# Optimization experiments

Measured on AMD Instinct MI355X. Metric: run time of the kernel, lower is better.

## Reference

```python
import jax, jax.numpy as jnp
import numpy as np

N_USERS = 70000
N_ITEMS = 30000
N_NODES = N_USERS + N_ITEMS
R = 3          # n_relations (hard-coded to 3 in original forward)
D = 64         # emb_dim
L = 2          # n_layers
E = 1_600_000  # nnz per relation adjacency


def setup_inputs() -> dict:
    key = jax.random.key(0)
    ks = jax.random.split(key, 11)
    s = 0.05  # xavier-ish scale
    return {
        'user_emb': jax.random.normal(ks[0], (N_USERS, D), jnp.float32) * s,
        'item_emb': jax.random.normal(ks[1], (N_ITEMS, D), jnp.float32) * s,
        'rel_emb':  jax.random.normal(ks[2], (R, D), jnp.float32) * s,
        'W_gc':     jax.random.normal(ks[3], (L, D, D), jnp.float32) * s,
        'W_rel':    jax.random.normal(ks[4], (L, D, D), jnp.float32) * s,
        'gru_w':    jax.random.normal(ks[5], (R, D, D), jnp.float32) * s,
        'gru_b':    jax.random.normal(ks[6], (R, D), jnp.float32) * s,
        'tra':      jax.random.normal(ks[7], (2, 2 * D), jnp.float32) * s,
        # normalized sparse adjacency values (~1/degree)
        'adj_vals': jax.random.uniform(ks[8], (R, E), jnp.float32) / 16.0,
        'adj_rows': jax.random.randint(ks[9], (R, E), 0, N_NODES, dtype=jnp.int32),
        'adj_cols': jax.random.randint(ks[10], (R, E), 0, N_NODES, dtype=jnp.int32),
    }


def reference(user_emb, item_emb, rel_emb, W_gc, W_rel, gru_w, gru_b, tra,
              adj_vals, adj_rows, adj_cols):
    # ego: [N, R, D] (same embedding replicated per relation channel)
    ego = jnp.broadcast_to(
        jnp.concatenate([user_emb, item_emb], axis=0)[:, None, :],
        (N_NODES, R, D))
    all_emb = ego
    rela = [rel_emb]  # per-layer relation embeddings [R, D]
    inv_sqrt = 1.0 / jnp.sqrt(jnp.float32(128.0))  # hard-coded in source

    for k in range(L):
        embs = []
        for i in range(R):  # small fixed relation loop
            # sparse adj @ ego[:, i, :] via gather + segment_sum
            msgs = ego[adj_cols[i], i, :] * adj_vals[i][:, None]        # [E, D]
            prop = jax.ops.segment_sum(msgs, adj_rows[i],
                                       num_segments=N_NODES)           # [N, D]
            embs.append(jax.nn.leaky_relu((prop * rela[k][i]) @ W_gc[k]))
        est = jnp.stack(embs, axis=1)                                   # [N, R, D]
        att = jax.nn.softmax(
            jnp.einsum('nrd,nsd->nrs', est, est) * inv_sqrt, axis=2)
        ego = jnp.einsum('nrs,nsd->nrd', att, est)
        # dropout rate 0.0 (eval) -> identity
        all_emb = all_emb + ego
        rela.append(rela[k] @ W_rel[k])

    att = jax.nn.softmax(jnp.einsum('nrd,nsd->nrs', all_emb, all_emb), axis=2)
    mid = jnp.einsum('nrs,nsd->nrd', att, all_emb)
    final = jnp.stack([all_emb[:, 0, :], all_emb[:, 1, :], mid[:, -1, :]],
                      axis=1) / (L + 1)                                  # [N, 3, D]
    u = final[:N_USERS]
    i_emb = jnp.concatenate(
        [final[N_USERS:], jnp.zeros((1, R, D), final.dtype)], axis=0)

    aux1 = u[:, 0, :] * (u[:, 0, :] @ gru_w[0] + gru_b[0])
    aux2 = u[:, 1, :] * (u[:, 1, :] @ gru_w[1] + gru_b[1])
    tgt = u[:, 2, :] * (u[:, 2, :] @ gru_w[2] + gru_b[2])
    score1 = jnp.concatenate([tgt, aux1], axis=1) @ tra[0]               # [N_u]
    score2 = jnp.concatenate([tgt, aux2], axis=1) @ tra[1]               # [N_u]

    rela_out = jnp.mean(jnp.stack(rela, axis=0), axis=0)                 # [R, D]
    return (u, i_emb, rela_out, score1, score2)
```

## Files before the change

### kernel.cpp

```cpp
#include <hip/hip_runtime.h>
#include <hip/hip_bf16.h>

#define N_USERS 70000
#define N_ITEMS 30000
#define N_NODES 100000
#define RD 192
#define EE 1600000
#define NE3 4800000
#define M3 300000
#define NSUB 98
#define NBUCK 294

#define OFF_U    0
#define OFF_I    13440000
#define OFF_IZ   19200000
#define OFF_RELA 19200192
#define OFF_S1   19200384
#define OFF_S2   19270384

typedef __hip_bfloat16 bf16;
typedef unsigned long long u64;
typedef __attribute__((ext_vector_type(8))) short short8;
typedef __attribute__((ext_vector_type(8))) unsigned short ushort8;
typedef __attribute__((ext_vector_type(4))) float f32x4;

__device__ __forceinline__ float b2f(bf16 v) { return __bfloat162float(v); }

union bfbits { bf16 b; unsigned short u; };

__device__ __forceinline__ float bits2f(unsigned short u) {
  bfbits x; x.u = u; return b2f(x.b);
}
__device__ __forceinline__ unsigned short f2bits(float f) {
  bfbits x; x.b = __float2bfloat16(f); return x.u;
}

__device__ __forceinline__ float loadf(const void* p, int i, bool f32) {
  return f32 ? ((const float*)p)[i] : b2f(((const bf16*)p)[i]);
}
__device__ __forceinline__ void storef(void* p, int i, float v, bool f32) {
  if (f32) ((float*)p)[i] = v;
  else ((bf16*)p)[i] = __float2bfloat16(v);
}

__device__ __forceinline__ float wave_sum(float v) {
#pragma unroll
  for (int off = 32; off >= 1; off >>= 1) v += __shfl_xor(v, off, 64);
  return v;
}

__global__ void detect_kernel(const unsigned short* __restrict__ ue,
                              int* __restrict__ flag) {
  __shared__ int s;
  int t = threadIdx.x;
  if (t == 0) s = 0;
  __syncthreads();
  int big = 0;
  for (int j = t; j < 8192; j += 256) {
    int e = (ue[j] >> 7) & 0xFF;
    if (e >= 127) big = 1;
  }
  if (big) atomicOr(&s, 1);
  __syncthreads();
  if (t == 0) *flag = s;
}

__global__ void zero_row_kernel(void* out, const int* __restrict__ flag) {
  bool f32 = *flag != 0;
  storef(out, OFF_IZ + (int)threadIdx.x, 0.f, f32);
}

__global__ void rela_kernel(const void* __restrict__ rel_emb,
                            const void* __restrict__ W_rel,
                            const int* __restrict__ flag,
                            float* __restrict__ rela_f, void* out) {
  bool f32 = *flag != 0;
  __shared__ float r0s[192], r1s[192];
  int t = threadIdx.x;
  int i = t >> 6, d = t & 63;
  float r0 = loadf(rel_emb, t, f32);
  r0s[t] = r0;
  __syncthreads();
  float acc = 0.f;
  for (int k = 0; k < 64; ++k)
    acc += r0s[i * 64 + k] * loadf(W_rel, k * 64 + d, f32);
  r1s[t] = acc;
  __syncthreads();
  float acc2 = 0.f;
  for (int k = 0; k < 64; ++k)
    acc2 += r1s[i * 64 + k] * loadf(W_rel, 4096 + k * 64 + d, f32);
  rela_f[t] = r0;
  rela_f[192 + t] = acc;
  rela_f[384 + t] = acc2;
  storef(out, OFF_RELA + t, (r0 + acc + acc2) * (1.f / 3.f), f32);
}

__global__ __launch_bounds__(256) void init_kernel(
    const void* __restrict__ user_emb, const void* __restrict__ item_emb,
    const int* __restrict__ flag, bf16* __restrict__ ego0) {
  bool f32 = *flag != 0;
  int idx4 = blockIdx.x * 256 + threadIdx.x;
  if (idx4 >= N_NODES * RD / 4) return;
  int idx = idx4 << 2;
  int n = idx / RD;
  int rd = idx - n * RD;
  int d = rd & 63;
  const void* src;
  int off;
  if (n < N_USERS) { src = user_emb; off = n * 64 + d; }
  else             { src = item_emb; off = (n - N_USERS) * 64 + d; }
  ushort4 o;
  if (f32) {
    float4 fv = *(const float4*)((const float*)src + off);
    o.x = f2bits(fv.x); o.y = f2bits(fv.y); o.z = f2bits(fv.z); o.w = f2bits(fv.w);
  } else {
    o = *(const ushort4*)((const unsigned short*)src + off);
  }
  *(ushort4*)(ego0 + idx) = o;
}

__global__ __launch_bounds__(256) void bhist_kernel(
    const int* __restrict__ rows, int* __restrict__ bcnt) {
  __shared__ int h[NBUCK];
  int t = threadIdx.x;
  for (int j = t; j < NBUCK; j += 256) h[j] = 0;
  __syncthreads();
  int base = blockIdx.x * 4096;
  int m = min(4096, NE3 - base);
  for (int j = t; j < m; j += 256) {
    int idx = base + j;
    int i = idx / EE;
    int r = rows[idx];
    atomicAdd(&h[i * NSUB + (r >> 10)], 1);
  }
  __syncthreads();
  for (int j = t; j < NBUCK; j += 256)
    if (h[j]) atomicAdd(&bcnt[j], h[j]);
}

__global__ __launch_bounds__(512) void bscan_kernel(
    const int* __restrict__ bcnt, int* __restrict__ gcursor,
    int* __restrict__ bbase) {
  __shared__ int s[512];
  int t = threadIdx.x;
  int x = (t < NBUCK) ? bcnt[t] : 0;
  s[t] = x;
  __syncthreads();
  for (int off = 1; off < 512; off <<= 1) {
    int y = (t >= off) ? s[t - off] : 0;
    __syncthreads();
    s[t] += y;
    __syncthreads();
  }
  if (t < NBUCK) {
    int e = s[t] - x;
    gcursor[t] = e;
    bbase[t] = e;
  }
}

__global__ __launch_bounds__(256) void passA_kernel(
    const int* __restrict__ rows, const int* __restrict__ cols,
    const void* __restrict__ vals, const int* __restrict__ flag,
    int* __restrict__ gcursor, u64* __restrict__ abuf) {
  bool f32 = *flag != 0;
  __shared__ u64 pk[4096];
  __shared__ unsigned short bk[4096];
  __shared__ int cnt[NBUCK], pos[NBUCK], gbase[NBUCK];
  int t = threadIdx.x;
  for (int j = t; j < NBUCK; j += 256) { cnt[j] = 0; pos[j] = 0; }
  __syncthreads();
  int base = blockIdx.x * 4096;
  int m = min(4096, NE3 - base);
  for (int j = t; j < m; j += 256) {
    int idx = base + j;
    int i = idx / EE;
    int r = rows[idx];
    int c = cols[idx];
    unsigned short vb =
        f32 ? f2bits(((const float*)vals)[idx])
            : ((const unsigned short*)vals)[idx];
    int sub = r >> 10;
    int b = i * NSUB + sub;
    pk[j] = ((u64)(r & 1023) << 48) | ((u64)(unsigned)c << 16) | vb;
    bk[j] = (unsigned short)b;
    atomicAdd(&cnt[b], 1);
  }
  __syncthreads();
  for (int j = t; j < NBUCK; j += 256)
    if (cnt[j] > 0) gbase[j] = atomicAdd(&gcursor[j], cnt[j]);
  __syncthreads();
  for (int j = t; j < m; j += 256) {
    int b = bk[j];
    int p = atomicAdd(&pos[b], 1);
    abuf[gbase[b] + p] = pk[j];
  }
}

__global__ __launch_bounds__(256) void passB_kernel(
    const u64* __restrict__ abuf, const int* __restrict__ bbase,
    const int* __restrict__ bcnt, int* __restrict__ offs,
    int* __restrict__ counts, int2* __restrict__ sedge) {
  __shared__ int hist[1024];
  __shared__ int s[256];
  int b = blockIdx.x;
  int rel = b / NSUB, sub = b - rel * NSUB;
  int r0 = sub << 10;
  int nr = min(1024, N_NODES - r0);
  int gi = rel * N_NODES + r0;
  int t = threadIdx.x;
  for (int j = t; j < 1024; j += 256) hist[j] = 0;
  __syncthreads();
  int start = bbase[b];
  int cnt = bcnt[b];
  int end = start + cnt;
  for (int e = start + t; e < end; e += 256)
    atomicAdd(&hist[(int)(abuf[e] >> 48)], 1);
  __syncthreads();
  int j0 = t << 2;
  int a0 = hist[j0], a1 = hist[j0 + 1], a2 = hist[j0 + 2], a3 = hist[j0 + 3];
  int lsum = a0 + a1 + a2 + a3;
  s[t] = lsum;
  __syncthreads();
  for (int off = 1; off < 256; off <<= 1) {
    int y = (t >= off) ? s[t - off] : 0;
    __syncthreads();
    s[t] += y;
    __syncthreads();
  }
  int o0 = start + s[t] - lsum;
  int o1 = o0 + a0, o2 = o1 + a1, o3 = o2 + a2;
  hist[j0] = o0; hist[j0 + 1] = o1; hist[j0 + 2] = o2; hist[j0 + 3] = o3;
  if (j0 < nr) {
    *(int4*)(offs + gi + j0) = make_int4(o0, o1, o2, o3);
    *(int4*)(counts + gi + j0) = make_int4(a0, a1, a2, a3);
  }
  __syncthreads();
  int rbase = rel * 128;
  for (int e = start + t; e < end; e += 256) {
    u64 w = abuf[e];
    int rowlo = (int)(w >> 48);
    int c = (int)((w >> 16) & 0x3FFFF);
    float v = bits2f((unsigned short)(w & 0xFFFF));
    int p = atomicAdd(&hist[rowlo], 1);
    int2 eo; eo.x = c * 384 + rbase; eo.y = __float_as_int(v);
    sedge[p] = eo;
  }
}

__global__ __launch_bounds__(256, 8) void gather_kernel(
    const int2* __restrict__ sedge, const int* __restrict__ counts,
    const int* __restrict__ offs, const bf16* __restrict__ ego,
    bf16* __restrict__ prop) {
  int wave = threadIdx.x >> 6;
  int n = blockIdx.x * 4 + wave;
  int rel = blockIdx.y;
  int seg = rel * N_NODES + n;
  int lane = threadIdx.x & 63;
  int g = lane >> 3;
  int d8 = lane & 7;
  unsigned voff = (unsigned)(d8 << 4);
  int base = __builtin_amdgcn_readfirstlane(offs[seg]);
  int cnt = __builtin_amdgcn_readfirstlane(counts[seg]);
  const char* egob = (const char*)ego;
  float a0 = 0.f, a1 = 0.f, a2 = 0.f, a3 = 0.f;
  float a4 = 0.f, a5 = 0.f, a6 = 0.f, a7 = 0.f;
#define ACCUM(dv, vv)                                          \
  do {                                                         \
    a0 = fmaf(__int_as_float((dv).x << 16), (vv), a0);         \
    a1 = fmaf(__int_as_float((dv).x & 0xffff0000u), (vv), a1); \
    a2 = fmaf(__int_as_float((dv).y << 16), (vv), a2);         \
    a3 = fmaf(__int_as_float((dv).y & 0xffff0000u), (vv), a3); \
    a4 = fmaf(__int_as_float((dv).z << 16), (vv), a4);         \
    a5 = fmaf(__int_as_float((dv).z & 0xffff0000u), (vv), a5); \
    a6 = fmaf(__int_as_float((dv).w << 16), (vv), a6);         \
    a7 = fmaf(__int_as_float((dv).w & 0xffff0000u), (vv), a7); \
  } while (0)
  int cm = cnt - 1;
  int nb = (cnt + 15) >> 4;
  int j = 0;
  if (nb & 1) {
    int iA = min(g, cm), iB = min(8 + g, cm);
    int2 h0 = sedge[base + iA];
    int2 h1 = sedge[base + iB];
    uint4 dA = *(const uint4*)(egob + ((unsigned)h0.x + voff));
    uint4 dB = *(const uint4*)(egob + ((unsigned)h1.x + voff));
    float v0 = (g < cnt) ? __int_as_float(h0.y) : 0.f;
    float v1 = (8 + g < cnt) ? __int_as_float(h1.y) : 0.f;
    ACCUM(dA, v0);
    ACCUM(dB, v1);
    j = 16;
  }
  int e16 = nb << 4;
  for (; j < e16; j += 32) {
    int iA0 = min(j + g, cm),      iB0 = min(j + 8 + g, cm);
    int iA1 = min(j + 16 + g, cm), iB1 = min(j + 24 + g, cm);
    int2 h0a = sedge[base + iA0];
    int2 h1a = sedge[base + iB0];
    int2 h0b = sedge[base + iA1];
    int2 h1b = sedge[base + iB1];
    uint4 dA = *(const uint4*)(egob + ((unsigned)h0a.x + voff));
    uint4 dB = *(const uint4*)(egob + ((unsigned)h1a.x + voff));
    uint4 dC = *(const uint4*)(egob + ((unsigned)h0b.x + voff));
    uint4 dD = *(const uint4*)(egob + ((unsigned)h1b.x + voff));
    float v0 = (j + g < cnt) ? __int_as_float(h0a.y) : 0.f;
    float v1 = (j + 8 + g < cnt) ? __int_as_float(h1a.y) : 0.f;
    float v2 = (j + 16 + g < cnt) ? __int_as_float(h0b.y) : 0.f;
    float v3 = (j + 24 + g < cnt) ? __int_as_float(h1b.y) : 0.f;
    ACCUM(dA, v0);
    ACCUM(dB, v1);
    ACCUM(dC, v2);
    ACCUM(dD, v3);
  }
#undef ACCUM
#pragma unroll
  for (int off = 8; off <= 32; off <<= 1) {
    a0 += __shfl_xor(a0, off, 64);
    a1 += __shfl_xor(a1, off, 64);
    a2 += __shfl_xor(a2, off, 64);
    a3 += __shfl_xor(a3, off, 64);
    a4 += __shfl_xor(a4, off, 64);
    a5 += __shfl_xor(a5, off, 64);
    a6 += __shfl_xor(a6, off, 64);
    a7 += __shfl_xor(a7, off, 64);
  }
  if (g == 0) {
    uint4 o;
    o.x = (unsigned)f2bits(a0) | ((unsigned)f2bits(a1) << 16);
    o.y = (unsigned)f2bits(a2) | ((unsigned)f2bits(a3) << 16);
    o.z = (unsigned)f2bits(a4) | ((unsigned)f2bits(a5) << 16);
    o.w = (unsigned)f2bits(a6) | ((unsigned)f2bits(a7) << 16);
    *(uint4*)((char*)prop + (size_t)(n * RD + rel * 64) * 2 + voff) = o;
  }
}

__device__ __forceinline__ float attn_row(float a, float b, float c,
                                          float e0, float e1, float e2) {
  float m = fmaxf(a, fmaxf(b, c));
  float w0 = __expf(a - m), w1 = __expf(b - m), w2 = __expf(c - m);
  float inv = 1.f / (w0 + w1 + w2);
  return (w0 * e0 + w1 * e1 + w2 * e2) * inv;
}

__global__ __launch_bounds__(256, 4) void transform_attn_kernel(
    const bf16* __restrict__ prop, const float* __restrict__ rela_k,
    const void* __restrict__ Wgc, int wgc_off, const int* __restrict__ flag,
    bf16* __restrict__ ego_out) {
  bool f32 = *flag != 0;
  __shared__ __align__(16) unsigned short est_t[64 * 198];
  int t = threadIdx.x, lane = t & 63, wave = t >> 6;
  int quad = lane >> 4, m = lane & 15;
  int wcol = wave * 16 + m;
  short8 b0, b1;
#pragma unroll
  for (int j = 0; j < 8; ++j) {
    int k0 = quad * 8 + j;
    b0[j] = (short)f2bits(loadf(Wgc, wgc_off + k0 * 64 + wcol, f32));
    b1[j] = (short)f2bits(loadf(Wgc, wgc_off + (k0 + 32) * 64 + wcol, f32));
  }
  float relv0[16], relv1[16], relv2[16];
#pragma unroll
  for (int j = 0; j < 8; ++j) {
    int k0 = quad * 8 + j;
    relv0[j] = rela_k[k0];        relv0[8 + j] = rela_k[32 + k0];
    relv1[j] = rela_k[64 + k0];   relv1[8 + j] = rela_k[96 + k0];
    relv2[j] = rela_k[128 + k0];  relv2[8 + j] = rela_k[160 + k0];
  }
  int n0 = blockIdx.x * 64;
  int row0 = n0 * 3;
#pragma unroll
  for (int tr = 0; tr < 12; ++tr) {
    int rl = tr * 16 + m;
    int row = row0 + rl;
    int row_c = row < M3 ? row : 0;
    int i = rl % 3;
    const ushort8* pp = (const ushort8*)(prop + (size_t)row_c * 64 + quad * 8);
    ushort8 x0 = pp[0];
    ushort8 x1 = pp[4];
    short8 a0, a1;
#pragma unroll
    for (int j = 0; j < 8; ++j) {
      float r0 = (i == 0) ? relv0[j] : (i == 1 ? relv1[j] : relv2[j]);
      float r1 = (i == 0) ? relv0[8 + j] : (i == 1 ? relv1[8 + j] : relv2[8 + j]);
      a0[j] = (short)f2bits(bits2f(x0[j]) * r0);
      a1[j] = (short)f2bits(bits2f(x1[j]) * r1);
    }
    f32x4 acc = {0.f, 0.f, 0.f, 0.f};
    acc = __builtin_amdgcn_mfma_f32_16x16x32_bf16(a0, b0, acc, 0, 0, 0);
    acc = __builtin_amdgcn_mfma_f32_16x16x32_bf16(a1, b1, acc, 0, 0, 0);
    float v0 = acc[0]; v0 = v0 > 0.f ? v0 : 0.01f * v0;
    float v1 = acc[1]; v1 = v1 > 0.f ? v1 : 0.01f * v1;
    float v2 = acc[2]; v2 = v2 > 0.f ? v2 : 0.01f * v2;
    float v3 = acc[3]; v3 = v3 > 0.f ? v3 : 0.01f * v3;
    unsigned w0 = (unsigned)f2bits(v0) | ((unsigned)f2bits(v1) << 16);
    unsigned w1 = (unsigned)f2bits(v2) | ((unsigned)f2bits(v3) << 16);
    unsigned* p32 = (unsigned*)(est_t + wcol * 198 + tr * 16 + quad * 4);
    p32[0] = w0; p32[1] = w1;
  }
  __syncthreads();
  const float sc = 0.088388347648318447f;
  for (int jj = 0; jj < 16; ++jj) {
    int nl = wave * 16 + jj;
    int n = n0 + nl;
    if (n >= N_NODES) break;
    int rb = lane * 198 + 3 * nl;
    float e0 = bits2f(est_t[rb]);
    float e1 = bits2f(est_t[rb + 1]);
    float e2 = bits2f(est_t[rb + 2]);
    float s00 = wave_sum(e0 * e0);
    float s01 = wave_sum(e0 * e1);
    float s02 = wave_sum(e0 * e2);
    float s11 = wave_sum(e1 * e1);
    float s12 = wave_sum(e1 * e2);
    float s22 = wave_sum(e2 * e2);
    float o0 = attn_row(s00 * sc, s01 * sc, s02 * sc, e0, e1, e2);
    float o1 = attn_row(s01 * sc, s11 * sc, s12 * sc, e0, e1, e2);
    float o2 = attn_row(s02 * sc, s12 * sc, s22 * sc, e0, e1, e2);
    int base = n * RD + lane;
    ego_out[base] = __float2bfloat16(o0);
    ego_out[base + 64] = __float2bfloat16(o1);
    ego_out[base + 128] = __float2bfloat16(o2);
  }
}

__global__ __launch_bounds__(256, 4) void final_kernel(
    const bf16* __restrict__ ego0, const bf16* __restrict__ ego1,
    const bf16* __restrict__ ego2, const void* __restrict__ gru_w,
    const void* __restrict__ gru_b, const void* __restrict__ tra,
    const int* __restrict__ flag, void* out) {
  bool f32 = *flag != 0;
  __shared__ __align__(16) unsigned short fmatu[192 * 72];
  __shared__ float sc_lds[128];
  int t = threadIdx.x, lane = t & 63, wave = t >> 6;
  int quad = lane >> 4, m = lane & 15;
  int wcol = wave * 16 + m;
  if (t < 128) sc_lds[t] = 0.f;
  short8 bw[3][2];
#pragma unroll
  for (int i = 0; i < 3; ++i)
#pragma unroll
    for (int j = 0; j < 8; ++j) {
      int k0 = quad * 8 + j;
      bw[i][0][j] = (short)f2bits(loadf(gru_w, i * 4096 + k0 * 64 + wcol, f32));
      bw[i][1][j] =
          (short)f2bits(loadf(gru_w, i * 4096 + (k0 + 32) * 64 + wcol, f32));
    }
  float bias0 = loadf(gru_b, wcol, f32);
  float bias1 = loadf(gru_b, 64 + wcol, f32);
  float bias2 = loadf(gru_b, 128 + wcol, f32);
  float ts0 = loadf(tra, wcol, f32);
  float ts1 = loadf(tra, 64 + wcol, f32);
  float ts2 = loadf(tra, 128 + wcol, f32);
  float ts3 = loadf(tra, 192 + wcol, f32);

  int n0 = blockIdx.x * 64;
  for (int jj = 0; jj < 16; ++jj) {
    int nl = wave * 16 + jj;
    int n = n0 + nl;
    float f0 = 0.f, f1 = 0.f, f2 = 0.f;
    if (n < N_NODES) {
      int b0i = n * RD + lane;
      float a0 = b2f(ego0[b0i]) + b2f(ego1[b0i]) + b2f(ego2[b0i]);
      float a1 =
          b2f(ego0[b0i + 64]) + b2f(ego1[b0i + 64]) + b2f(ego2[b0i + 64]);
      float a2 =
          b2f(ego0[b0i + 128]) + b2f(ego1[b0i + 128]) + b2f(ego2[b0i + 128]);
      float s20 = wave_sum(a2 * a0);
      float s21 = wave_sum(a2 * a1);
      float s22 = wave_sum(a2 * a2);
      float mid2 = attn_row(s20, s21, s22, a0, a1, a2);
      f0 = a0 * (1.f / 3.f);
      f1 = a1 * (1.f / 3.f);
      f2 = mid2 * (1.f / 3.f);
      if (n < N_USERS) {
        int ob = OFF_U + n * RD + lane;
        storef(out, ob, f0, f32);
        storef(out, ob + 64, f1, f32);
        storef(out, ob + 128, f2, f32);
      } else {
        int ob = OFF_I + (n - N_USERS) * RD + lane;
        storef(out, ob, f0, f32);
        storef(out, ob + 64, f1, f32);
        storef(out, ob + 128, f2, f32);
      }
    }
    fmatu[(0 * 64 + nl) * 72 + lane] = f2bits(f0);
    fmatu[(1 * 64 + nl) * 72 + lane] = f2bits(f1);
    fmatu[(2 * 64 + nl) * 72 + lane] = f2bits(f2);
  }
  __syncthreads();
  float p1a[4][4], p2a[4][4];
#pragma unroll
  for (int tr = 0; tr < 4; ++tr)
#pragma unroll
    for (int r = 0; r < 4; ++r) { p1a[tr][r] = 0.f; p2a[tr][r] = 0.f; }
#pragma unroll
  for (int i = 0; i < 3; ++i) {
    float bias = (i == 0) ? bias0 : (i == 1 ? bias1 : bias2);
#pragma unroll
    for (int tr = 0; tr < 4; ++tr) {
      int arow = (i * 64 + tr * 16 + m) * 72;
      short8 a0 = *(const short8*)(fmatu + arow + quad * 8);
      short8 a1 = *(const short8*)(fmatu + arow + 32 + quad * 8);
      f32x4 acc = {0.f, 0.f, 0.f, 0.f};
      acc = __builtin_amdgcn_mfma_f32_16x16x32_bf16(a0, bw[i][0], acc, 0, 0, 0);
      acc = __builtin_amdgcn_mfma_f32_16x16x32_bf16(a1, bw[i][1], acc, 0, 0, 0);
#pragma unroll
      for (int r = 0; r < 4; ++r) {
        int nl = tr * 16 + quad * 4 + r;
        float y = acc[r] + bias;
        float f = bits2f(fmatu[(i * 64 + nl) * 72 + wcol]);
        float prod = f * y;
        if (i == 0) p1a[tr][r] += prod * ts1;
        else if (i == 1) p2a[tr][r] += prod * ts3;
        else { p1a[tr][r] += prod * ts0; p2a[tr][r] += prod * ts2; }
      }
    }
  }
#pragma unroll
  for (int tr = 0; tr < 4; ++tr)
#pragma unroll
    for (int r = 0; r < 4; ++r) {
      float p1 = p1a[tr][r], p2 = p2a[tr][r];
#pragma unroll
      for (int off = 1; off < 16; off <<= 1) {
        p1 += __shfl_xor(p1, off, 64);
        p2 += __shfl_xor(p2, off, 64);
      }
      if (m == 0) {
        int nl = tr * 16 + quad * 4 + r;
        atomicAdd(&sc_lds[nl * 2], p1);
        atomicAdd(&sc_lds[nl * 2 + 1], p2);
      }
    }
  __syncthreads();
  if (t < 64) {
    int n = n0 + t;
    if (n < N_USERS) {
      storef(out, OFF_S1 + n, sc_lds[t * 2], f32);
      storef(out, OFF_S2 + n, sc_lds[t * 2 + 1], f32);
    }
  }
}

extern "C" void kernel_launch(void* const* d_in, const int* in_sizes, int n_in,
                              void* d_out, int out_size, void* d_ws,
                              size_t ws_size, hipStream_t stream) {
  const void* user_emb = d_in[0];
  const void* item_emb = d_in[1];
  const void* rel_emb = d_in[2];
  const void* W_gc = d_in[3];
  const void* W_rel = d_in[4];
  const void* gru_w = d_in[5];
  const void* gru_b = d_in[6];
  const void* tra = d_in[7];
  const void* adj_vals = d_in[8];
  const int* adj_rows = (const int*)d_in[9];
  const int* adj_cols = (const int*)d_in[10];

  int* flag = (int*)d_ws;
  float* wsf = (float*)d_ws;
  float* rela_f = wsf + 16;
  int* counts = (int*)(wsf + 1024);
  int* offs = counts + M3;
  int* gcursor = offs + M3;
  int* bcnt = gcursor + 512;
  int* bbase = bcnt + 512;
  u64* abuf = (u64*)(bbase + 512);
  int2* sedge = (int2*)(abuf + NE3);
  bf16* ego0 = (bf16*)(sedge + NE3);
  bf16* ego1 = ego0 + (size_t)N_NODES * RD;
  bf16* ego2 = ego1 + (size_t)N_NODES * RD;
  bf16* prop = ego2 + (size_t)N_NODES * RD;

  const int nbE = (NE3 + 4095) / 4096;

  detect_kernel<<<1, 256, 0, stream>>>((const unsigned short*)user_emb, flag);
  rela_kernel<<<1, 192, 0, stream>>>(rel_emb, W_rel, flag, rela_f, d_out);
  zero_row_kernel<<<1, 192, 0, stream>>>(d_out, flag);
  init_kernel<<<(N_NODES * RD / 4 + 255) / 256, 256, 0, stream>>>(
      user_emb, item_emb, flag, ego0);

  (void)hipMemsetAsync(bcnt, 0, 512 * sizeof(int), stream);
  bhist_kernel<<<nbE, 256, 0, stream>>>(adj_rows, bcnt);
  bscan_kernel<<<1, 512, 0, stream>>>(bcnt, gcursor, bbase);
  passA_kernel<<<nbE, 256, 0, stream>>>(
      adj_rows, adj_cols, adj_vals, flag, gcursor, abuf);
  passB_kernel<<<NBUCK, 256, 0, stream>>>(abuf, bbase, bcnt, offs, counts,
                                          sedge);

  gather_kernel<<<dim3(N_NODES / 4, 3), 256, 0, stream>>>(
      sedge, counts, offs, ego0, prop);
  transform_attn_kernel<<<(N_NODES + 63) / 64, 256, 0, stream>>>(
      prop, rela_f, W_gc, 0, flag, ego1);
  gather_kernel<<<dim3(N_NODES / 4, 3), 256, 0, stream>>>(
      sedge, counts, offs, ego1, prop);
  transform_attn_kernel<<<(N_NODES + 63) / 64, 256, 0, stream>>>(
      prop, rela_f + 192, W_gc, 4096, flag, ego2);

  final_kernel<<<(N_NODES + 63) / 64, 256, 0, stream>>>(
      ego0, ego1, ego2, gru_w, gru_b, tra, flag, d_out);
}
```

Before: 735.0 us.

## Store prop relation-major, fold rela into W_gc, use 512-thread blocks

The gather kernel now writes prop in relation-major layout ([R][N][64]) instead of node-interleaved. The transform kernel uses this to feed prop rows straight into MFMA without the per-element rela scaling, which is instead folded into per-relation pre-scaled weight fragments. Both the transform and final kernels go to 512-thread blocks, with two wave groups splitting the 64-node tile so each wave handles fewer nodes. The extra per-relation weight registers and the larger blocks may raise register pressure. Rounding also changes slightly, because rela*W is now rounded to bf16 rather than prop*rela.

```diff
diff --git a/kernel.cpp b/kernel.cpp
--- a/kernel.cpp
+++ b/kernel.cpp
@@ -330,7 +330,7 @@
     o.y = (unsigned)f2bits(a2) | ((unsigned)f2bits(a3) << 16);
     o.z = (unsigned)f2bits(a4) | ((unsigned)f2bits(a5) << 16);
     o.w = (unsigned)f2bits(a6) | ((unsigned)f2bits(a7) << 16);
-    *(uint4*)((char*)prop + (size_t)(n * RD + rel * 64) * 2 + voff) = o;
+    *(uint4*)((char*)prop + (((size_t)rel * N_NODES + n) << 7) + voff) = o;
   }
 }
 
@@ -342,7 +342,7 @@
   return (w0 * e0 + w1 * e1 + w2 * e2) * inv;
 }
 
-__global__ __launch_bounds__(256, 4) void transform_attn_kernel(
+__global__ __launch_bounds__(512, 6) void transform_attn_kernel(
     const bf16* __restrict__ prop, const float* __restrict__ rela_k,
     const void* __restrict__ Wgc, int wgc_off, const int* __restrict__ flag,
     bf16* __restrict__ ego_out) {
@@ -350,63 +350,57 @@
   __shared__ __align__(16) unsigned short est_t[64 * 198];
   int t = threadIdx.x, lane = t & 63, wave = t >> 6;
   int quad = lane >> 4, m = lane & 15;
-  int wcol = wave * 16 + m;
-  short8 b0, b1;
-#pragma unroll
-  for (int j = 0; j < 8; ++j) {
-    int k0 = quad * 8 + j;
-    b0[j] = (short)f2bits(loadf(Wgc, wgc_off + k0 * 64 + wcol, f32));
-    b1[j] = (short)f2bits(loadf(Wgc, wgc_off + (k0 + 32) * 64 + wcol, f32));
-  }
-  float relv0[16], relv1[16], relv2[16];
-#pragma unroll
-  for (int j = 0; j < 8; ++j) {
-    int k0 = quad * 8 + j;
-    relv0[j] = rela_k[k0];        relv0[8 + j] = rela_k[32 + k0];
-    relv1[j] = rela_k[64 + k0];   relv1[8 + j] = rela_k[96 + k0];
-    relv2[j] = rela_k[128 + k0];  relv2[8 + j] = rela_k[160 + k0];
-  }
+  int wcol = (wave & 3) * 16 + m;
+  short8 bw[3][2];
+#pragma unroll
+  for (int i = 0; i < 3; ++i)
+#pragma unroll
+    for (int j = 0; j < 8; ++j) {
+      int k0 = quad * 8 + j;
+      bw[i][0][j] = (short)f2bits(
+          rela_k[i * 64 + k0] * loadf(Wgc, wgc_off + k0 * 64 + wcol, f32));
+      bw[i][1][j] = (short)f2bits(
+          rela_k[i * 64 + k0 + 32] *
+          loadf(Wgc, wgc_off + (k0 + 32) * 64 + wcol, f32));
+    }
   int n0 = blockIdx.x * 64;
-  int row0 = n0 * 3;
-#pragma unroll
-  for (int tr = 0; tr < 12; ++tr) {
-    int rl = tr * 16 + m;
-    int row = row0 + rl;
-    int row_c = row < M3 ? row : 0;
-    int i = rl % 3;
-    const ushort8* pp = (const ushort8*)(prop + (size_t)row_c * 64 + quad * 8);
-    ushort8 x0 = pp[0];
-    ushort8 x1 = pp[4];
-    short8 a0, a1;
-#pragma unroll
-    for (int j = 0; j < 8; ++j) {
-      float r0 = (i == 0) ? relv0[j] : (i == 1 ? relv1[j] : relv2[j]);
-      float r1 = (i == 0) ? relv0[8 + j] : (i == 1 ? relv1[8 + j] : relv2[8 + j]);
-      a0[j] = (short)f2bits(bits2f(x0[j]) * r0);
-      a1[j] = (short)f2bits(bits2f(x1[j]) * r1);
-    }
-    f32x4 acc = {0.f, 0.f, 0.f, 0.f};
-    acc = __builtin_amdgcn_mfma_f32_16x16x32_bf16(a0, b0, acc, 0, 0, 0);
-    acc = __builtin_amdgcn_mfma_f32_16x16x32_bf16(a1, b1, acc, 0, 0, 0);
-    float v0 = acc[0]; v0 = v0 > 0.f ? v0 : 0.01f * v0;
-    float v1 = acc[1]; v1 = v1 > 0.f ? v1 : 0.01f * v1;
-    float v2 = acc[2]; v2 = v2 > 0.f ? v2 : 0.01f * v2;
-    float v3 = acc[3]; v3 = v3 > 0.f ? v3 : 0.01f * v3;
-    unsigned w0 = (unsigned)f2bits(v0) | ((unsigned)f2bits(v1) << 16);
-    unsigned w1 = (unsigned)f2bits(v2) | ((unsigned)f2bits(v3) << 16);
-    unsigned* p32 = (unsigned*)(est_t + wcol * 198 + tr * 16 + quad * 4);
-    p32[0] = w0; p32[1] = w1;
-  }
+#define DO_TILE(TR)                                                           \
+  {                                                                           \
+    constexpr int rel_ = (TR) >> 2;                                           \
+    int node = n0 + (((TR) & 3) << 4) + m;                                    \
+    if (node > N_NODES - 1) node = N_NODES - 1;                               \
+    const short8* pp = (const short8*)(prop +                                 \
+        ((size_t)rel_ * N_NODES + node) * 64 + quad * 8);                     \
+    short8 x0 = pp[0];                                                        \
+    short8 x1 = pp[4];                                                        \
+    f32x4 acc = {0.f, 0.f, 0.f, 0.f};                                         \
+    acc = __builtin_amdgcn_mfma_f32_16x16x32_bf16(x0, bw[rel_][0], acc, 0, 0, 0); \
+    acc = __builtin_amdgcn_mfma_f32_16x16x32_bf16(x1, bw[rel_][1], acc, 0, 0, 0); \
+    float v0 = acc[0]; v0 = v0 > 0.f ? v0 : 0.01f * v0;                       \
+    float v1 = acc[1]; v1 = v1 > 0.f ? v1 : 0.01f * v1;                       \
+    float v2 = acc[2]; v2 = v2 > 0.f ? v2 : 0.01f * v2;                       \
+    float v3 = acc[3]; v3 = v3 > 0.f ? v3 : 0.01f * v3;                       \
+    unsigned w0 = (unsigned)f2bits(v0) | ((unsigned)f2bits(v1) << 16);        \
+    unsigned w1 = (unsigned)f2bits(v2) | ((unsigned)f2bits(v3) << 16);        \
+    unsigned* p32 = (unsigned*)(est_t + wcol * 198 + (TR) * 16 + quad * 4);   \
+    p32[0] = w0; p32[1] = w1;                                                 \
+  }
+  if ((wave >> 2) == 0) {
+    DO_TILE(0) DO_TILE(1) DO_TILE(2) DO_TILE(3) DO_TILE(4) DO_TILE(5)
+  } else {
+    DO_TILE(6) DO_TILE(7) DO_TILE(8) DO_TILE(9) DO_TILE(10) DO_TILE(11)
+  }
+#undef DO_TILE
   __syncthreads();
   const float sc = 0.088388347648318447f;
-  for (int jj = 0; jj < 16; ++jj) {
-    int nl = wave * 16 + jj;
+  for (int jj = 0; jj < 8; ++jj) {
+    int nl = wave * 8 + jj;
     int n = n0 + nl;
     if (n >= N_NODES) break;
-    int rb = lane * 198 + 3 * nl;
+    int rb = lane * 198 + nl;
     float e0 = bits2f(est_t[rb]);
-    float e1 = bits2f(est_t[rb + 1]);
-    float e2 = bits2f(est_t[rb + 2]);
+    float e1 = bits2f(est_t[rb + 64]);
+    float e2 = bits2f(est_t[rb + 128]);
     float s00 = wave_sum(e0 * e0);
     float s01 = wave_sum(e0 * e1);
     float s02 = wave_sum(e0 * e2);
@@ -423,7 +417,7 @@
   }
 }
 
-__global__ __launch_bounds__(256, 4) void final_kernel(
+__global__ __launch_bounds__(512, 6) void final_kernel(
     const bf16* __restrict__ ego0, const bf16* __restrict__ ego1,
     const bf16* __restrict__ ego2, const void* __restrict__ gru_w,
     const void* __restrict__ gru_b, const void* __restrict__ tra,
@@ -433,7 +427,7 @@
   __shared__ float sc_lds[128];
   int t = threadIdx.x, lane = t & 63, wave = t >> 6;
   int quad = lane >> 4, m = lane & 15;
-  int wcol = wave * 16 + m;
+  int wcol = (wave & 3) * 16 + m;
   if (t < 128) sc_lds[t] = 0.f;
   short8 bw[3][2];
 #pragma unroll
@@ -454,8 +448,8 @@
   float ts3 = loadf(tra, 192 + wcol, f32);
 
   int n0 = blockIdx.x * 64;
-  for (int jj = 0; jj < 16; ++jj) {
-    int nl = wave * 16 + jj;
+  for (int jj = 0; jj < 8; ++jj) {
+    int nl = wave * 8 + jj;
     int n = n0 + nl;
     float f0 = 0.f, f1 = 0.f, f2 = 0.f;
     if (n < N_NODES) {
@@ -489,16 +483,18 @@
     fmatu[(2 * 64 + nl) * 72 + lane] = f2bits(f2);
   }
   __syncthreads();
-  float p1a[4][4], p2a[4][4];
-#pragma unroll
-  for (int tr = 0; tr < 4; ++tr)
-#pragma unroll
-    for (int r = 0; r < 4; ++r) { p1a[tr][r] = 0.f; p2a[tr][r] = 0.f; }
+  int trbase = (wave >> 2) * 2;
+  float p1a[2][4], p2a[2][4];
+#pragma unroll
+  for (int tt = 0; tt < 2; ++tt)
+#pragma unroll
+    for (int r = 0; r < 4; ++r) { p1a[tt][r] = 0.f; p2a[tt][r] = 0.f; }
 #pragma unroll
   for (int i = 0; i < 3; ++i) {
     float bias = (i == 0) ? bias0 : (i == 1 ? bias1 : bias2);
 #pragma unroll
-    for (int tr = 0; tr < 4; ++tr) {
+    for (int tt = 0; tt < 2; ++tt) {
+      int tr = trbase + tt;
       int arow = (i * 64 + tr * 16 + m) * 72;
       short8 a0 = *(const short8*)(fmatu + arow + quad * 8);
       short8 a1 = *(const short8*)(fmatu + arow + 32 + quad * 8);
@@ -511,24 +507,24 @@
         float y = acc[r] + bias;
         float f = bits2f(fmatu[(i * 64 + nl) * 72 + wcol]);
         float prod = f * y;
-        if (i == 0) p1a[tr][r] += prod * ts1;
-        else if (i == 1) p2a[tr][r] += prod * ts3;
-        else { p1a[tr][r] += prod * ts0; p2a[tr][r] += prod * ts2; }
+        if (i == 0) p1a[tt][r] += prod * ts1;
+        else if (i == 1) p2a[tt][r] += prod * ts3;
+        else { p1a[tt][r] += prod * ts0; p2a[tt][r] += prod * ts2; }
       }
     }
   }
 #pragma unroll
-  for (int tr = 0; tr < 4; ++tr)
+  for (int tt = 0; tt < 2; ++tt)
 #pragma unroll
     for (int r = 0; r < 4; ++r) {
-      float p1 = p1a[tr][r], p2 = p2a[tr][r];
+      float p1 = p1a[tt][r], p2 = p2a[tt][r];
 #pragma unroll
       for (int off = 1; off < 16; off <<= 1) {
         p1 += __shfl_xor(p1, off, 64);
         p2 += __shfl_xor(p2, off, 64);
       }
       if (m == 0) {
-        int nl = tr * 16 + quad * 4 + r;
+        int nl = (trbase + tt) * 16 + quad * 4 + r;
         atomicAdd(&sc_lds[nl * 2], p1);
         atomicAdd(&sc_lds[nl * 2 + 1], p2);
       }
@@ -591,13 +587,13 @@
 
   gather_kernel<<<dim3(N_NODES / 4, 3), 256, 0, stream>>>(
       sedge, counts, offs, ego0, prop);
-  transform_attn_kernel<<<(N_NODES + 63) / 64, 256, 0, stream>>>(
+  transform_attn_kernel<<<(N_NODES + 63) / 64, 512, 0, stream>>>(
       prop, rela_f, W_gc, 0, flag, ego1);
   gather_kernel<<<dim3(N_NODES / 4, 3), 256, 0, stream>>>(
       sedge, counts, offs, ego1, prop);
-  transform_attn_kernel<<<(N_NODES + 63) / 64, 256, 0, stream>>>(
+  transform_attn_kernel<<<(N_NODES + 63) / 64, 512, 0, stream>>>(
       prop, rela_f + 192, W_gc, 4096, flag, ego2);
 
-  final_kernel<<<(N_NODES + 63) / 64, 256, 0, stream>>>(
+  final_kernel<<<(N_NODES + 63) / 64, 512, 0, stream>>>(
       ego0, ego1, ego2, gru_w, gru_b, tra, flag, d_out);
 }
```

Result: slower. 831.9 us (+13.2%).
